# Optimization experiments

Hardware: AMD Instinct MI355X
Metric: run time of the kernel (lower is better)

## Reference

```python
import jax, jax.numpy as jnp
import numpy as np

N = 500_000
D = 256  # input_dim
H = 256  # hidden_dim
CLAMP = 10.0


def setup_inputs() -> dict:
    key = jax.random.key(0)
    ks = jax.random.split(key, 7)
    inputs = jax.random.normal(ks[0], (N, D), dtype=jnp.float32)
    query = jax.random.normal(ks[1], (D,), dtype=jnp.float32)
    mask = jax.random.randint(ks[2], (N,), 0, 2, dtype=jnp.int32)
    # nn.Linear(in, out, bias=False).weight has shape (out, in); scale like torch default
    s = 1.0 / np.sqrt(D)
    W_query = jax.random.uniform(ks[3], (H, D), jnp.float32, -s, s)
    W_key = jax.random.uniform(ks[4], (H, D), jnp.float32, -s, s)
    W_value = jax.random.uniform(ks[5], (H, D), jnp.float32, -s, s)
    sh = 1.0 / np.sqrt(H)
    W_out = jax.random.uniform(ks[6], (H,), jnp.float32, -sh, sh)
    return {"inputs": inputs, "query": query, "mask": mask,
            "W_query": W_query, "W_key": W_key, "W_value": W_value, "W_out": W_out}


def reference(inputs, query, mask, W_query, W_key, W_value, W_out):
    # Q: [H], K,V: [N,H]
    Q = W_query @ query
    K = jnp.einsum('nd,hd->nh', inputs, W_key)
    V = jnp.einsum('nd,hd->nh', inputs, W_value)
    scale = jnp.sqrt(jnp.asarray(H, dtype=inputs.dtype))
    scores = (K @ Q) / scale                      # [N]
    scores = jnp.where(mask == 0, -jnp.inf, scores)
    weights = jax.nn.softmax(scores, axis=-1)     # [N]
    attended = weights[:, None] * V               # [N,H] (elementwise, no sum)
    logits = attended @ W_out                     # [N]
    return CLAMP * jnp.tanh(logits)
```

## Files before the change

kernel.cpp:

```cpp
#include <hip/hip_runtime.h>
#include <math.h>

typedef float f4 __attribute__((ext_vector_type(4)));
typedef float f2 __attribute__((ext_vector_type(2)));

#define DIM 256
#define NF4 64
#define NB_MAIN 2048

__device__ inline float dot4(f4 a, f4 b) {
  return a.x * b.x + a.y * b.y + a.z * b.z + a.w * b.w;
}

__device__ inline void sm_combine(float& m, float& l, float bm, float bl) {
  float mn = fmaxf(m, bm);
  float e1 = (l  != 0.f) ? __expf(m  - mn) : 0.f;
  float e2 = (bl != 0.f) ? __expf(bm - mn) : 0.f;
  l = l * e1 + bl * e2;
  m = mn;
}

__global__ void qba_prep(const float* __restrict__ Wq,
                         const float* __restrict__ query,
                         const float* __restrict__ Wk,
                         const float* __restrict__ Wv,
                         const float* __restrict__ Wout,
                         float* __restrict__ q_eff,
                         float* __restrict__ v_eff) {
  __shared__ float Qs[DIM];
  __shared__ float part[4][DIM];
  int tid = threadIdx.x;
  int q = tid >> 8, d = tid & 255;
  if (blockIdx.x == 0) {
    int lane = tid & 63, w = tid >> 6;
    f4 qv = reinterpret_cast<const f4*>(query)[lane];
    #pragma unroll 4
    for (int i = 0; i < 16; ++i) {
      int h = w * 16 + i;
      f4 wv = reinterpret_cast<const f4*>(Wq + (size_t)h * DIM)[lane];
      float acc = dot4(wv, qv);
      #pragma unroll
      for (int off = 32; off > 0; off >>= 1) acc += __shfl_xor(acc, off);
      if (lane == 0) Qs[h] = acc;
    }
    __syncthreads();
    float a = 0.f;
    #pragma unroll 16
    for (int i = 0; i < 64; ++i) {
      int h = q * 64 + i;
      a += Wk[(size_t)h * DIM + d] * Qs[h];
    }
    part[q][d] = a;
    __syncthreads();
    if (tid < DIM)
      q_eff[tid] = (part[0][tid] + part[1][tid] + part[2][tid] + part[3][tid]) * 0.0625f;
  } else {
    float a = 0.f;
    #pragma unroll 16
    for (int i = 0; i < 64; ++i) {
      int h = q * 64 + i;
      a += Wv[(size_t)h * DIM + d] * Wout[h];
    }
    part[q][d] = a;
    __syncthreads();
    if (tid < DIM)
      v_eff[tid] = part[0][tid] + part[1][tid] + part[2][tid] + part[3][tid];
  }
}

__global__ void __launch_bounds__(256)
qba_main(const float* __restrict__ inputs,
         const int* __restrict__ mask,
         const float* __restrict__ q_eff,
         const float* __restrict__ v_eff,
         f2* __restrict__ st_buf,
         float* __restrict__ block_m,
         float* __restrict__ block_l,
         int N) {
  int lane = threadIdx.x & 63;
  int wid  = threadIdx.x >> 6;
  int g    = lane >> 4;
  int sub  = lane & 15;
  const f4* in4 = reinterpret_cast<const f4*>(inputs);

  f4 qe[4], ve[4];
  #pragma unroll
  for (int k = 0; k < 4; ++k) {
    qe[k] = reinterpret_cast<const f4*>(q_eff)[sub + 16 * k];
    ve[k] = reinterpret_cast<const f4*>(v_eff)[sub + 16 * k];
  }

  int wave   = blockIdx.x * 4 + wid;
  const int stride = NB_MAIN * 16;
  float m = -INFINITY, l = 0.f;

  for (int n0 = wave * 4; n0 < N; n0 += stride) {
    int row  = n0 + g;
    int rowc = row < N ? row : N - 1;
    const f4* rp = in4 + (size_t)rowc * NF4 + sub;
    f4 x0 = __builtin_nontemporal_load(rp);
    f4 x1 = __builtin_nontemporal_load(rp + 16);
    f4 x2 = __builtin_nontemporal_load(rp + 32);
    f4 x3 = __builtin_nontemporal_load(rp + 48);
    int mk = mask[rowc];

    float s = dot4(x0, qe[0]) + dot4(x1, qe[1]) + dot4(x2, qe[2]) + dot4(x3, qe[3]);
    float t = dot4(x0, ve[0]) + dot4(x1, ve[1]) + dot4(x2, ve[2]) + dot4(x3, ve[3]);
    #pragma unroll
    for (int off = 1; off < 16; off <<= 1) {
      s += __shfl_xor(s, off);
      t += __shfl_xor(t, off);
    }

    if (row < N) {
      if (sub == 0) {
        f2 v; v.x = mk ? s : -INFINITY; v.y = t;
        st_buf[row] = v;
      }
      if (mk) {
        float mn = fmaxf(m, s);
        l = l * __expf(m - mn) + __expf(s - mn);
        m = mn;
      }
    }
  }

  #pragma unroll
  for (int off = 16; off < 64; off <<= 1) {
    float bm = __shfl_xor(m, off);
    float bl = __shfl_xor(l, off);
    sm_combine(m, l, bm, bl);
  }

  __shared__ float sm[4], sl[4];
  if (lane == 0) { sm[wid] = m; sl[wid] = l; }
  __syncthreads();
  if (threadIdx.x == 0) {
    float M = sm[0], L = sl[0];
    #pragma unroll
    for (int i = 1; i < 4; ++i) sm_combine(M, L, sm[i], sl[i]);
    block_m[blockIdx.x] = M;
    block_l[blockIdx.x] = L;
  }
}

__global__ void __launch_bounds__(256)
qba_final(const f2* __restrict__ st,
          const float* __restrict__ block_m,
          const float* __restrict__ block_l,
          f4* __restrict__ out4, int N4) {
  int tid = threadIdx.x;
  int lane = tid & 63, wid = tid >> 6;

  float m = -INFINITY, l = 0.f;
  #pragma unroll
  for (int k = 0; k < NB_MAIN / 256; ++k) {
    int i = tid + k * 256;
    sm_combine(m, l, block_m[i], block_l[i]);
  }
  #pragma unroll
  for (int off = 32; off > 0; off >>= 1) {
    float bm = __shfl_xor(m, off);
    float bl = __shfl_xor(l, off);
    sm_combine(m, l, bm, bl);
  }
  __shared__ float sm[4], sl[4];
  __shared__ float MSs[2];
  if (lane == 0) { sm[wid] = m; sl[wid] = l; }
  __syncthreads();
  if (tid == 0) {
    float M = sm[0], L = sl[0];
    #pragma unroll
    for (int i = 1; i < 4; ++i) sm_combine(M, L, sm[i], sl[i]);
    MSs[0] = M;
    MSs[1] = 1.f / L;
  }
  __syncthreads();

  int i = blockIdx.x * 256 + tid;
  if (i >= N4) return;
  float M = MSs[0], invS = MSs[1];
  const f4* st4 = reinterpret_cast<const f4*>(st);
  f4 a = st4[2 * i];
  f4 b = st4[2 * i + 1];
  f4 r;
  r.x = 10.f * tanhf(__expf(a.x - M) * invS * a.y);
  r.y = 10.f * tanhf(__expf(a.z - M) * invS * a.w);
  r.z = 10.f * tanhf(__expf(b.x - M) * invS * b.y);
  r.w = 10.f * tanhf(__expf(b.z - M) * invS * b.w);
  out4[i] = r;
}

extern "C" void kernel_launch(void* const* d_in, const int* in_sizes, int n_in,
                              void* d_out, int out_size, void* d_ws, size_t ws_size,
                              hipStream_t stream) {
  const float* inputs = (const float*)d_in[0];
  const float* query  = (const float*)d_in[1];
  const int*   mask   = (const int*)d_in[2];
  const float* Wq     = (const float*)d_in[3];
  const float* Wk     = (const float*)d_in[4];
  const float* Wv     = (const float*)d_in[5];
  const float* Wout   = (const float*)d_in[6];
  float* out = (float*)d_out;
  int N = in_sizes[2];

  float* ws     = (float*)d_ws;
  f2*    st_buf = (f2*)ws;
  float* q_eff  = ws + 2 * N;
  float* v_eff  = q_eff + DIM;
  float* bm     = v_eff + DIM;
  float* bl     = bm + NB_MAIN;

  qba_prep <<<2, 1024, 0, stream>>>(Wq, query, Wk, Wv, Wout, q_eff, v_eff);
  qba_main <<<NB_MAIN, 256, 0, stream>>>(inputs, mask, q_eff, v_eff,
                                         st_buf, bm, bl, N);
  qba_final<<<(N / 4 + 255) / 256, 256, 0, stream>>>(
      st_buf, bm, bl, (f4*)out, N / 4);
}
```

Measured before the change: 93.94 us.

## Fuse main pass and finalize into cooperative kernel with grid-wide sync

Replaces the separate main and final kernels with one cooperative kernel. Each block processes a contiguous chunk of rows, keeps the (score, value) pairs in shared memory, and computes a local softmax max/sum. A grid.sync then lets every block combine the global max/sum and write its own outputs. This removes the global round-trip of the intermediate buffer and one kernel launch. In exchange it adds host-side device attribute and occupancy queries, a grid-wide barrier, and a fixed shared-memory buffer that may limit occupancy.

```diff
diff --git a/kernel.cpp b/kernel.cpp
--- a/kernel.cpp
+++ b/kernel.cpp
@@ -1,5 +1,8 @@
 #include <hip/hip_runtime.h>
+#include <hip/hip_cooperative_groups.h>
 #include <math.h>
+
+namespace cg = cooperative_groups;
 
 typedef float f4 __attribute__((ext_vector_type(4)));
 typedef float f2 __attribute__((ext_vector_type(2)));
@@ -7,6 +10,7 @@
 #define DIM 256
 #define NF4 64
 #define NB_MAIN 2048
+#define MAX_CHUNK 2048
 
 __device__ inline float dot4(f4 a, f4 b) {
   return a.x * b.x + a.y * b.y + a.z * b.z + a.w * b.w;
@@ -68,6 +72,115 @@
   }
 }
 
+__global__ void __launch_bounds__(256, 4)
+qba_fused(const float* __restrict__ inputs,
+          const int* __restrict__ mask,
+          const float* __restrict__ q_eff,
+          const float* __restrict__ v_eff,
+          float* __restrict__ block_m,
+          float* __restrict__ block_l,
+          float* __restrict__ out,
+          int N, int chunk) {
+  __shared__ f2 st[MAX_CHUNK];
+  __shared__ float sm[4], sl[4], MSs[2];
+
+  int tid  = threadIdx.x;
+  int lane = tid & 63;
+  int wid  = tid >> 6;
+  int g    = lane >> 4;
+  int sub  = lane & 15;
+  int base = blockIdx.x * chunk;
+  const f4* in4 = reinterpret_cast<const f4*>(inputs);
+
+  f4 qe[4], ve[4];
+  #pragma unroll
+  for (int k = 0; k < 4; ++k) {
+    qe[k] = reinterpret_cast<const f4*>(q_eff)[sub + 16 * k];
+    ve[k] = reinterpret_cast<const f4*>(v_eff)[sub + 16 * k];
+  }
+
+  int nrows = N - base;
+  int lim = nrows < chunk ? nrows : chunk;
+
+  float m = -INFINITY, l = 0.f;
+  for (int l0 = 0; l0 < lim; l0 += 16) {
+    int lrow = l0 + wid * 4 + g;
+    int row  = base + lrow;
+    int rowc = row < N ? row : N - 1;
+    const f4* rp = in4 + (size_t)rowc * NF4 + sub;
+    f4 x0 = __builtin_nontemporal_load(rp);
+    f4 x1 = __builtin_nontemporal_load(rp + 16);
+    f4 x2 = __builtin_nontemporal_load(rp + 32);
+    f4 x3 = __builtin_nontemporal_load(rp + 48);
+    int mk = mask[rowc];
+
+    float s = dot4(x0, qe[0]) + dot4(x1, qe[1]) + dot4(x2, qe[2]) + dot4(x3, qe[3]);
+    float t = dot4(x0, ve[0]) + dot4(x1, ve[1]) + dot4(x2, ve[2]) + dot4(x3, ve[3]);
+    #pragma unroll
+    for (int off = 1; off < 16; off <<= 1) {
+      s += __shfl_xor(s, off);
+      t += __shfl_xor(t, off);
+    }
+
+    if (row < N && lrow < lim) {
+      if (sub == 0) {
+        f2 v; v.x = mk ? s : -INFINITY; v.y = t;
+        st[lrow] = v;
+      }
+      if (mk) {
+        float mn = fmaxf(m, s);
+        l = l * __expf(m - mn) + __expf(s - mn);
+        m = mn;
+      }
+    }
+  }
+
+  #pragma unroll
+  for (int off = 16; off < 64; off <<= 1) {
+    float bm = __shfl_xor(m, off);
+    float bl = __shfl_xor(l, off);
+    sm_combine(m, l, bm, bl);
+  }
+  if (lane == 0) { sm[wid] = m; sl[wid] = l; }
+  __syncthreads();
+  if (tid == 0) {
+    float M = sm[0], L = sl[0];
+    #pragma unroll
+    for (int i = 1; i < 4; ++i) sm_combine(M, L, sm[i], sl[i]);
+    block_m[blockIdx.x] = M;
+    block_l[blockIdx.x] = L;
+    __threadfence();
+  }
+
+  cg::this_grid().sync();
+
+  float cm = -INFINITY, cl = 0.f;
+  for (int i = tid; i < (int)gridDim.x; i += 256)
+    sm_combine(cm, cl, block_m[i], block_l[i]);
+  #pragma unroll
+  for (int off = 32; off > 0; off >>= 1) {
+    float bm = __shfl_xor(cm, off);
+    float bl = __shfl_xor(cl, off);
+    sm_combine(cm, cl, bm, bl);
+  }
+  if (lane == 0) { sm[wid] = cm; sl[wid] = cl; }
+  __syncthreads();
+  if (tid == 0) {
+    float M = sm[0], L = sl[0];
+    #pragma unroll
+    for (int i = 1; i < 4; ++i) sm_combine(M, L, sm[i], sl[i]);
+    MSs[0] = M;
+    MSs[1] = 1.f / L;
+  }
+  __syncthreads();
+
+  float M = MSs[0], invS = MSs[1];
+  for (int lr = tid; lr < lim; lr += 256) {
+    f2 v = st[lr];
+    out[base + lr] = 10.f * tanhf(__expf(v.x - M) * invS * v.y);
+  }
+}
+
 __global__ void __launch_bounds__(256)
 qba_main(const float* __restrict__ inputs,
          const int* __restrict__ mask,
@@ -131,7 +244,6 @@
     float bl = __shfl_xor(l, off);
     sm_combine(m, l, bm, bl);
   }
-
   __shared__ float sm[4], sl[4];
   if (lane == 0) { sm[wid] = m; sl[wid] = l; }
   __syncthreads();
@@ -206,14 +318,34 @@
 
   float* ws     = (float*)d_ws;
   f2*    st_buf = (f2*)ws;
-  float* q_eff  = ws + 2 * N;
+  float* q_eff  = ws + 2 * (size_t)N;
   float* v_eff  = q_eff + DIM;
   float* bm     = v_eff + DIM;
   float* bl     = bm + NB_MAIN;
 
-  qba_prep <<<2, 1024, 0, stream>>>(Wq, query, Wk, Wv, Wout, q_eff, v_eff);
-  qba_main <<<NB_MAIN, 256, 0, stream>>>(inputs, mask, q_eff, v_eff,
-                                         st_buf, bm, bl, N);
-  qba_final<<<(N / 4 + 255) / 256, 256, 0, stream>>>(
-      st_buf, bm, bl, (f4*)out, N / 4);
-}
+  qba_prep<<<2, 1024, 0, stream>>>(Wq, query, Wk, Wv, Wout, q_eff, v_eff);
+
+  int dev = 0;
+  hipGetDevice(&dev);
+  int cus = 0, coop = 0, maxB = 0;
+  hipDeviceGetAttribute(&cus,  hipDeviceAttributeMultiprocessorCount, dev);
+  hipDeviceGetAttribute(&coop, hipDeviceAttributeCooperativeLaunch,   dev);
+  hipError_t qerr = hipOccupancyMaxActiveBlocksPerMultiprocessor(&maxB, qba_fused, 256, 0);
+
+  long cap = (long)maxB * (long)cus;
+  if (coop && qerr == hipSuccess && cap >= 320) {
+    int grid = cap > NB_MAIN ? NB_MAIN : (int)cap;
+    int chunk = ((N + grid - 1) / grid + 15) & ~15;
+    if (chunk > MAX_CHUNK) chunk = MAX_CHUNK;
+    grid = (N + chunk - 1) / chunk;
+    void* args[] = { (void*)&inputs, (void*)&mask, (void*)&q_eff, (void*)&v_eff,
+                     (void*)&bm, (void*)&bl, (void*)&out, (void*)&N, (void*)&chunk };
+    hipLaunchCooperativeKernel((const void*)qba_fused, dim3(grid), dim3(256),
+                               args, 0, stream);
+  } else {
+    qba_main <<<NB_MAIN, 256, 0, stream>>>(inputs, mask, q_eff, v_eff,
+                                           st_buf, bm, bl, N);
+    qba_final<<<(N / 4 + 255) / 256, 256, 0, stream>>>(
+        st_buf, bm, bl, (f4*)out, N / 4);
+  }
+}
```

Result: slower. 220.2 us (+134.4%).
